# Optimization experiments

Hardware: AMD Instinct MI355X
Metric: run time of the kernel (lower is better)

The kernel has to match this reference:

```python
import jax, jax.numpy as jnp
import numpy as np

B, S, D, H, DK, DFF, L = 4, 1024, 1024, 16, 64, 4096, 128

def setup_inputs() -> dict:
    key = jax.random.key(0)
    ks = jax.random.split(key, 20)
    stdv = 1.0 / np.sqrt(D)
    u = lambda k, shape, s=stdv: jax.random.uniform(k, shape, jnp.float32, -s, s)
    x = jax.random.normal(ks[0], (B, S, D), jnp.float32)
    causal = jnp.triu(jnp.ones((S, S), bool), 1)          # True = masked
    attn_mask = jnp.broadcast_to(causal, (B, S, S))
    return {
        "x": x,
        "attn_mask": attn_mask,
        "W_q": u(ks[1], (H * DK, D)), "b_q": jnp.zeros((H * DK,)),
        "W_k": u(ks[2], (H * DK, D)), "b_k": jnp.zeros((H * DK,)),
        "W_v": u(ks[3], (H * DK, D)), "b_v": jnp.zeros((H * DK,)),
        "W_o": u(ks[4], (D, H * DK)), "b_o": jnp.zeros((D,)),
        "W_rel": u(ks[5], (2 * L + 1, DK), 1.0 / np.sqrt(DK)),
        "ln1_alpha": jnp.ones((D,)), "ln1_bias": jnp.zeros((D,)),
        "ln2_alpha": jnp.ones((D,)), "ln2_bias": jnp.zeros((D,)),
        "W1": u(ks[6], (DFF, D)), "b1": jnp.zeros((DFF,)),
        "W2": u(ks[7], (D, DFF)), "b2": jnp.zeros((D,)),
    }

def _layer_norm(x, alpha, bias, eps=1e-5):
    # Faithful to source: (x - mean) / (std + eps), std is biased (unbiased=False)
    m = jnp.mean(x, axis=-1, keepdims=True)
    std = jnp.sqrt(jnp.mean((x - m) ** 2, axis=-1, keepdims=True))
    return alpha * (x - m) / (std + eps) + bias

def reference(x, attn_mask, W_q, b_q, W_k, b_k, W_v, b_v, W_o, b_o, W_rel,
              ln1_alpha, ln1_bias, ln2_alpha, ln2_bias, W1, b1, W2, b2):
    b, s, d = x.shape
    q = (x @ W_q.T + b_q).reshape(b, s, H, DK)
    k = (x @ W_k.T + b_k).reshape(b, s, H, DK)
    v = (x @ W_v.T + b_v).reshape(b, s, H, DK)
    # relative position bias table lookup -> [s, s, DK]
    idx = jnp.clip(jnp.arange(s)[:, None] - jnp.arange(s)[None, :], -L, L) + L
    pos = W_rel[idx]
    # NOTE: original uses rel_pos_k_emb for BOTH pos_key and pos_value (as in source).
    scores = jnp.einsum('bqnd,bknd->bnqk', q, k) + jnp.einsum('bqnd,qkd->bnqk', q, pos)
    scores = scores / np.sqrt(DK)
    scores = jnp.where(attn_mask[:, None, :, :], jnp.float32(-10000.0), scores)
    attn = jax.nn.softmax(scores, axis=-1)
    out = jnp.einsum('bnqk,bknd->bnqd', attn, v) + jnp.einsum('bnqk,qkd->bnqd', attn, pos)
    out = out.transpose(0, 2, 1, 3).reshape(b, s, H * DK)
    out = out @ W_o.T + b_o
    # post-LN transformer layer: LN(x + attn), then LN(h + FFN(h))
    h = _layer_norm(x + out, ln1_alpha, ln1_bias)
    f = jax.nn.relu(h @ W1.T + b1) @ W2.T + b2
    return _layer_norm(h + f, ln2_alpha, ln2_bias)
```

## Files before the change

### kernel.cpp

```cpp
#include <hip/hip_runtime.h>
#include <cmath>
#include <cstdint>

typedef __bf16 bf16;
typedef __bf16 bf16x8 __attribute__((ext_vector_type(8)));
typedef __bf16 bf16x4 __attribute__((ext_vector_type(4)));
typedef float f32x4 __attribute__((ext_vector_type(4)));

#define CEXP 0.1803368852f

__device__ __forceinline__ void async_ld16(const void* g, void* l) {
  __builtin_amdgcn_global_load_lds(
      (__attribute__((address_space(1))) void*)(uintptr_t)g,
      (__attribute__((address_space(3))) void*)l, 16, 0, 0);
}

__global__ __launch_bounds__(256) void cast_all(
    const float* __restrict__ x,  const float* __restrict__ wq, const float* __restrict__ wk,
    const float* __restrict__ wv, const float* __restrict__ wo, const float* __restrict__ w1,
    const float* __restrict__ w2,
    bf16* xb, bf16* wqb, bf16* wkb, bf16* wvb, bf16* wob, bf16* w1b, bf16* w2b)
{
  int i = blockIdx.x * 256 + threadIdx.x;
  const int M1 = 1 << 20, Q = 1 << 18;
  const float* src; bf16* dst; int off;
  if      (i < M1)            { src = x;  dst = xb;  off = i; }
  else if (i < M1 + Q)        { src = wq; dst = wqb; off = i - M1; }
  else if (i < M1 + 2 * Q)    { src = wk; dst = wkb; off = i - M1 - Q; }
  else if (i < M1 + 3 * Q)    { src = wv; dst = wvb; off = i - M1 - 2 * Q; }
  else if (i < M1 + 4 * Q)    { src = wo; dst = wob; off = i - M1 - 3 * Q; }
  else if (i < 3 * M1)        { src = w1; dst = w1b; off = i - M1 - 4 * Q; }
  else                        { src = w2; dst = w2b; off = i - 3 * M1; }
  float4 v = ((const float4*)src)[off];
  bf16x4 o; o[0]=(bf16)v.x; o[1]=(bf16)v.y; o[2]=(bf16)v.z; o[3]=(bf16)v.w;
  ((bf16x4*)dst)[off] = o;
}

template<int BM>
__device__ __forceinline__ void gemm_core(
    const bf16* __restrict__ A, const bf16* __restrict__ Bm, const float* __restrict__ bias,
    float* __restrict__ outF, bf16* __restrict__ outB,
    const float* __restrict__ residF, const bf16* __restrict__ residB,
    int N, int kld, int kbeg, int kend, int relu, bf16* As, bf16* Bs)
{
  constexpr int MI = BM / 32;
  const int tid  = threadIdx.x;
  const int wave = tid >> 6, lane = tid & 63;
  const int lr = lane & 15, lq = lane >> 4;
  const int bm = blockIdx.x * BM, bn = blockIdx.y * 128;
  const int wm = (wave >> 1) * (BM / 2), wn = (wave & 1) * 64;
  const int srow = lane >> 2, scol = (lane & 3) * 8;

  const f32x4 fz = {0.f, 0.f, 0.f, 0.f};
  f32x4 acc[MI][4];
#pragma unroll
  for (int i = 0; i < MI; i++)
#pragma unroll
    for (int j = 0; j < 4; j++) acc[i][j] = fz;

  auto issue = [&](int k0, int buf) {
    bf16* Ad = As + buf * (BM * 32);
    bf16* Bd = Bs + buf * (128 * 32);
    if (BM == 128) {
#pragma unroll
      for (int cc = 0; cc < 2; ++cc) {
        int c = wave * 2 + cc;
        async_ld16(A + (size_t)(bm + c * 16 + srow) * kld + k0 + scol, Ad + c * 512);
      }
    } else {
      async_ld16(A + (size_t)(bm + wave * 16 + srow) * kld + k0 + scol, Ad + wave * 512);
    }
#pragma unroll
    for (int cc = 0; cc < 2; ++cc) {
      int c = wave * 2 + cc;
      async_ld16(Bm + (size_t)(bn + c * 16 + srow) * kld + k0 + scol, Bd + c * 512);
    }
  };

  const int nit = (kend - kbeg) >> 5;
  issue(kbeg, 0);
  for (int i = 0; i < nit; i++) {
    __syncthreads();
    if (i + 1 < nit) issue(kbeg + (i + 1) * 32, (i + 1) & 1);
    const bf16* Ab = As + (i & 1) * (BM * 32);
    const bf16* Bb = Bs + (i & 1) * (128 * 32);
    bf16x8 af[MI], bfr[4];
#pragma unroll
    for (int mi = 0; mi < MI; mi++) af[mi]  = *(const bf16x8*)(Ab + (wm + mi*16 + lr)*32 + lq*8);
#pragma unroll
    for (int ni = 0; ni < 4; ni++) bfr[ni] = *(const bf16x8*)(Bb + (wn + ni*16 + lr)*32 + lq*8);
#pragma unroll
    for (int mi = 0; mi < MI; mi++)
#pragma unroll
      for (int ni = 0; ni < 4; ni++)
        acc[mi][ni] = __builtin_amdgcn_mfma_f32_16x16x32_bf16(af[mi], bfr[ni], acc[mi][ni], 0, 0, 0);
  }

#pragma unroll
  for (int ni = 0; ni < 4; ni++) {
    int n = bn + wn + ni*16 + lr;
    float bv = bias ? bias[n] : 0.0f;
#pragma unroll
    for (int mi = 0; mi < MI; mi++) {
#pragma unroll
      for (int r = 0; r < 4; r++) {
        int m = bm + wm + mi*16 + lq*4 + r;
        size_t idx = (size_t)m * N + n;
        float v = acc[mi][ni][r] + bv;
        if (relu) v = fmaxf(v, 0.0f);
        if (residF) v += residF[idx];
        if (residB) v += (float)residB[idx];
        if (outF) outF[idx] = v;
        else      outB[idx] = (bf16)v;
      }
    }
  }
}

__global__ __launch_bounds__(256) void gemm_splitk(
    const bf16* A, const bf16* Bm, float* part, int N, int kld, int kchunk)
{
  __shared__ bf16 As[2 * 128 * 32];
  __shared__ bf16 Bs[2 * 128 * 32];
  const int z = blockIdx.z;
  gemm_core<128>(A, Bm, nullptr, part + (size_t)z * 4096 * N, nullptr, nullptr, nullptr,
                 N, kld, z * kchunk, (z + 1) * kchunk, 0, As, Bs);
}

__device__ __forceinline__ void gemm256_core(
    const bf16* __restrict__ A, const bf16* __restrict__ Bm,
    const float* __restrict__ bias, bf16* __restrict__ outB,
    int N, int K, int relu, bf16* As, bf16* Bs)
{
  const int tid  = threadIdx.x;
  const int wave = tid >> 6, lane = tid & 63;
  const int lr = lane & 15, lq = lane >> 4;
  const int bm = blockIdx.x * 256, bn = blockIdx.y * 256;
  const int wm = (wave >> 2) * 128, wn = (wave & 3) * 64;

  const f32x4 fz = {0.f, 0.f, 0.f, 0.f};
  f32x4 acc[8][4];
#pragma unroll
  for (int i = 0; i < 8; ++i)
#pragma unroll
    for (int j = 0; j < 4; ++j) acc[i][j] = fz;

  int srow[4], scol[4];
#pragma unroll
  for (int L = 0; L < 4; ++L) {
    int cidx = L * 512 + wave * 64 + lane;
    srow[L] = cidx >> 3;
    scol[L] = ((cidx & 7) ^ (srow[L] & 7)) * 8;
  }

  auto issue = [&](int kt, int buf) {
    const int k0 = kt * 64;
#pragma unroll
    for (int L = 0; L < 4; ++L)
      async_ld16(A + (size_t)(bm + srow[L]) * K + k0 + scol[L],
                 As + buf * (256 * 64) + (L * 512 + wave * 64) * 8);
#pragma unroll
    for (int L = 0; L < 4; ++L)
      async_ld16(Bm + (size_t)(bn + srow[L]) * K + k0 + scol[L],
                 Bs + buf * (256 * 64) + (L * 512 + wave * 64) * 8);
  };

  const int NT = K >> 6;
  issue(0, 0);
  issue(1, 1);
  asm volatile("s_waitcnt vmcnt(8)" ::: "memory");
  __builtin_amdgcn_sched_barrier(0);
  __builtin_amdgcn_s_barrier();

  for (int t = 0; t < NT; ++t) {
    const bf16* Ab = As + (t & 1) * (256 * 64);
    const bf16* Bb = Bs + (t & 1) * (256 * 64);
#pragma unroll
    for (int mh = 0; mh < 2; ++mh) {
      bf16x8 af[4][2];
#pragma unroll
      for (int mi = 0; mi < 4; ++mi) {
        int row = wm + mh * 64 + mi * 16 + lr;
#pragma unroll
        for (int ks = 0; ks < 2; ++ks)
          af[mi][ks] = *(const bf16x8*)(Ab + row * 64 + (((ks * 4 + lq) ^ (lr & 7)) * 8));
      }
#pragma unroll
      for (int nh = 0; nh < 2; ++nh) {
        bf16x8 bfr[2][2];
#pragma unroll
        for (int ni = 0; ni < 2; ++ni) {
          int row = wn + nh * 32 + ni * 16 + lr;
#pragma unroll
          for (int ks = 0; ks < 2; ++ks)
            bfr[ni][ks] = *(const bf16x8*)(Bb + row * 64 + (((ks * 4 + lq) ^ (lr & 7)) * 8));
        }
        __builtin_amdgcn_s_setprio(1);
#pragma unroll
        for (int mi = 0; mi < 4; ++mi)
#pragma unroll
          for (int ni = 0; ni < 2; ++ni)
#pragma unroll
            for (int ks = 0; ks < 2; ++ks)
              acc[mh * 4 + mi][nh * 2 + ni] = __builtin_amdgcn_mfma_f32_16x16x32_bf16(
                  af[mi][ks], bfr[ni][ks], acc[mh * 4 + mi][nh * 2 + ni], 0, 0, 0);
        __builtin_amdgcn_s_setprio(0);
      }
    }
    if (t + 1 == NT) break;
    asm volatile("s_waitcnt lgkmcnt(0)" ::: "memory");
    __builtin_amdgcn_sched_barrier(0);
    __builtin_amdgcn_s_barrier();
    if (t + 2 < NT) {
      issue(t + 2, t & 1);
      asm volatile("s_waitcnt vmcnt(8)" ::: "memory");
    } else {
      asm volatile("s_waitcnt vmcnt(0)" ::: "memory");
    }
    __builtin_amdgcn_sched_barrier(0);
    __builtin_amdgcn_s_barrier();
  }

#pragma unroll
  for (int mi8 = 0; mi8 < 8; ++mi8) {
#pragma unroll
    for (int ni4 = 0; ni4 < 4; ++ni4) {
      int n = bn + wn + ni4 * 16 + lr;
      float bv = bias ? bias[n] : 0.0f;
#pragma unroll
      for (int r = 0; r < 4; ++r) {
        int m = bm + wm + mi8 * 16 + lq * 4 + r;
        float v = acc[mi8][ni4][r] + bv;
        if (relu) v = fmaxf(v, 0.0f);
        outB[(size_t)m * N + n] = (bf16)v;
      }
    }
  }
}

__global__ __launch_bounds__(512) void gemm256(
    const bf16* __restrict__ A, const bf16* __restrict__ Bm,
    const float* __restrict__ bias, bf16* __restrict__ outB,
    int N, int K, int relu)
{
  __shared__ __align__(16) bf16 As[2 * 256 * 64];
  __shared__ __align__(16) bf16 Bs[2 * 256 * 64];
  gemm256_core(A, Bm, bias, outB, N, K, relu, As, Bs);
}

__global__ __launch_bounds__(512) void gemm256_qkv(
    const bf16* __restrict__ A, const bf16* __restrict__ Bq, const bf16* __restrict__ Bk,
    const bf16* __restrict__ Bv, const float* __restrict__ bq, const float* __restrict__ bk,
    const float* __restrict__ bv, bf16* Oq, bf16* Ok, bf16* Ov, int N, int K)
{
  __shared__ __align__(16) bf16 As[2 * 256 * 64];
  __shared__ __align__(16) bf16 Bs[2 * 256 * 64];
  const bf16* Bm  = blockIdx.z == 0 ? Bq : (blockIdx.z == 1 ? Bk : Bv);
  const float* bi = blockIdx.z == 0 ? bq : (blockIdx.z == 1 ? bk : bv);
  bf16* O         = blockIdx.z == 0 ? Oq : (blockIdx.z == 1 ? Ok : Ov);
  gemm256_core(A, Bm, bi, O, N, K, 0, As, Bs);
}

__global__ __launch_bounds__(256) void transpose_v(const bf16* __restrict__ V, bf16* __restrict__ Vt) {
  __shared__ bf16 t[64][72];
  const int tid = threadIdx.x;
  const int sblk = blockIdx.x;
  const int bh = blockIdx.y;
  const int b = bh >> 4, h = bh & 15;
  const int sr = tid >> 2, dc = (tid & 3) * 16;
  const bf16* src = V + ((size_t)(b * 1024 + sblk * 64 + sr)) * 1024 + h * 64 + dc;
  bf16x8 r0 = *(const bf16x8*)src;
  bf16x8 r1 = *(const bf16x8*)(src + 8);
  *(bf16x8*)(&t[sr][dc]) = r0;
  *(bf16x8*)(&t[sr][dc + 8]) = r1;
  __syncthreads();
  const int dr = tid >> 2, sc = (tid & 3) * 16;
  bf16 o[16];
#pragma unroll
  for (int j = 0; j < 16; j++) o[j] = t[sc + j][dr];
  bf16* dst = Vt + ((size_t)(bh * 64 + dr)) * 1024 + sblk * 64 + sc;
  *(bf16x8*)dst = *(bf16x8*)&o[0];
  *(bf16x8*)(dst + 8) = *(bf16x8*)&o[8];
}

#define S_LEN 1024
#define ROWSTR 1024

__global__ __launch_bounds__(256) void attn_kernel(
    const bf16* __restrict__ Qg, const bf16* __restrict__ Kg, const bf16* __restrict__ Vt,
    const float* __restrict__ Wrel, bf16* __restrict__ Og)
{
  __shared__ __align__(16) bf16 hist[64][136];
  __shared__ __align__(16) bf16 rel_s[64][132];
  __shared__ __align__(16) bf16 ovl[8704];
  bf16* V_T  = ovl;
  bf16* Pb   = ovl + 4096;
  bf16* Wst  = ovl;
  bf16* Wr_t = ovl;
  float* lbuf = (float*)rel_s;
  float* hbuf = lbuf + 256;

  const int tid = threadIdx.x;
  const int wave = tid >> 6, lane = tid & 63;
  const int lr = lane & 15, lq = lane >> 4;
  const int qblk = 15 - blockIdx.y;
  const int bh = blockIdx.x;
  const int b = bh >> 4, h = bh & 15;
  const int q0 = qblk * 64;
  const int T = qblk + 1;
  const int nearStart = (T > 3) ? T - 3 : 0;
  const size_t rowbase = (size_t)b * S_LEN * ROWSTR + h * 64;
  const size_t vtbase = (size_t)(bh * 64) * 1024;
  const f32x4 fz = {0.f, 0.f, 0.f, 0.f};

  for (int e = tid; e < 2048; e += 256) {
    float4 v = ((const float4*)(Wrel + 8192))[e];
    bf16x4 o; o[0]=(bf16)v.x; o[1]=(bf16)v.y; o[2]=(bf16)v.z; o[3]=(bf16)v.w;
    ((bf16x4*)Wst)[e] = o;
  }
  {
    uint4 z4 = {0u, 0u, 0u, 0u};
    for (int e = tid; e < 1088; e += 256) ((uint4*)hist)[e] = z4;
  }

  bf16x8 qf[4][2];
#pragma unroll
  for (int qt = 0; qt < 4; qt++)
#pragma unroll
    for (int c = 0; c < 2; c++)
      qf[qt][c] = *(const bf16x8*)(Qg + rowbase + (size_t)(q0 + qt*16 + lr) * ROWSTR + c*32 + lq*8);

  bf16x8 wb[2];
#pragma unroll
  for (int c = 0; c < 2; c++)
#pragma unroll
    for (int j = 0; j < 8; j++)
      wb[c][j] = (bf16)Wrel[(size_t)256 * 64 + c*32 + lq*8 + j];

  __syncthreads();

#pragma unroll
  for (int tt = 0; tt < 2; ++tt)
#pragma unroll
    for (int qt = 0; qt < 4; ++qt) {
      f32x4 a = fz;
#pragma unroll
      for (int c = 0; c < 2; c++) {
        bf16x8 wf = *(const bf16x8*)(Wst + (wave*32 + tt*16 + lr) * 64 + c*32 + lq*8);
        a = __builtin_amdgcn_mfma_f32_16x16x32_bf16(wf, qf[qt][c], a, 0, 0, 0);
      }
      bf16x4 pk; pk[0]=(bf16)(a[0]*CEXP); pk[1]=(bf16)(a[1]*CEXP);
                 pk[2]=(bf16)(a[2]*CEXP); pk[3]=(bf16)(a[3]*CEXP);
      *(bf16x4*)(&rel_s[qt*16 + lr][wave*32 + tt*16 + lq*4]) = pk;
    }
  {
    f32x4 a = fz;
#pragma unroll
    for (int c = 0; c < 2; c++)
      a = __builtin_amdgcn_mfma_f32_16x16x32_bf16(wb[c], qf[wave][c], a, 0, 0, 0);
    if (lq == 0) rel_s[wave*16 + lr][128] = (bf16)(a[0]*CEXP);
  }
  __syncthreads();

  float relc[4];
#pragma unroll
  for (int qt = 0; qt < 4; qt++) relc[qt] = (float)rel_s[qt*16 + lr][128];

  float l_p[4] = {0.f,0.f,0.f,0.f}, h_p[4] = {0.f,0.f,0.f,0.f};
  f32x4 acc_o[4];
#pragma unroll
  for (int dt = 0; dt < 4; dt++) acc_o[dt] = fz;

  const int vd1 = tid >> 3;
  const int vj  = (tid & 7) ^ (vd1 & 7);
  const int krow = 16 * wave + lr;

  uint4 va, vb, va2, vb2;
  bf16x8 kf0, kf1, kn0, kn1;
  {
    const bf16* vp = Vt + vtbase + (size_t)vd1 * 1024 + vj * 8;
    va = *(const uint4*)vp; vb = *(const uint4*)(vp + 32 * 1024);
    const bf16* kp = Kg + rowbase + (size_t)krow * ROWSTR + lq*8;
    kf0 = *(const bf16x8*)kp; kf1 = *(const bf16x8*)(kp + 32);
  }

  for (int kt = 0; kt < T; ++kt) {
    const int k0 = kt * 64;

    f32x4 sc[4];
#pragma unroll
    for (int qt = 0; qt < 4; qt++) {
      sc[qt] = __builtin_amdgcn_mfma_f32_16x16x32_bf16(kf0, qf[qt][0], fz, 0, 0, 0);
      sc[qt] = __builtin_amdgcn_mfma_f32_16x16x32_bf16(kf1, qf[qt][1], sc[qt], 0, 0, 0);
    }
    if (kt + 1 < T) {
      const bf16* vp = Vt + vtbase + (size_t)vd1 * 1024 + k0 + 64 + vj * 8;
      va2 = *(const uint4*)vp; vb2 = *(const uint4*)(vp + 32 * 1024);
      const bf16* kp = Kg + rowbase + (size_t)(k0 + 64 + krow) * ROWSTR + lq*8;
      kn0 = *(const bf16x8*)kp; kn1 = *(const bf16x8*)(kp + 32);
    }

    float pw[4][4];
    if (kt < nearStart) {
#pragma unroll
      for (int qt = 0; qt < 4; qt++) {
#pragma unroll
        for (int r = 0; r < 4; r++) pw[qt][r] = exp2f(fmaf(sc[qt][r], CEXP, relc[qt]));
        float s4 = pw[qt][0] + pw[qt][1] + pw[qt][2] + pw[qt][3];
        l_p[qt] += s4; h_p[qt] += s4;
      }
    } else {
#pragma unroll
      for (int qt = 0; qt < 4; qt++) {
        int qg = q0 + qt*16 + lr;
#pragma unroll
        for (int r = 0; r < 4; r++) {
          int kg = k0 + 16*wave + lq*4 + r;
          float p = 0.0f;
          if (kg <= qg) {
            int t = qg - kg; int tc = t > 128 ? 128 : t;
            p = exp2f(fmaf(sc[qt][r], CEXP, (float)rel_s[qt*16 + lr][tc]));
            l_p[qt] += p;
            if (t >= 128) h_p[qt] += p;
            else          hist[qt*16 + lr][t] = (bf16)p;
          }
          pw[qt][r] = p;
        }
      }
    }

    __syncthreads();
    *(uint4*)(V_T + tid * 8) = va;
    *(uint4*)(V_T + (tid + 256) * 8) = vb;
#pragma unroll
    for (int qt = 0; qt < 4; qt++) {
      bf16x4 pk; pk[0]=(bf16)pw[qt][0]; pk[1]=(bf16)pw[qt][1];
                 pk[2]=(bf16)pw[qt][2]; pk[3]=(bf16)pw[qt][3];
      *(bf16x4*)(Pb + (qt*16 + lr) * 72 + 16*wave + lq*4) = pk;
    }
    __syncthreads();

#pragma unroll
    for (int c = 0; c < 2; c++) {
      bf16x8 pf = *(const bf16x8*)(Pb + (16*wave + lr) * 72 + c*32 + lq*8);
#pragma unroll
      for (int dt = 0; dt < 4; dt++) {
        int vd = dt*16 + lr;
        int jx = (c*4 + lq) ^ (vd & 7);
        bf16x8 vf = *(const bf16x8*)(V_T + ((vd << 3) + jx) * 8);
        acc_o[dt] = __builtin_amdgcn_mfma_f32_16x16x32_bf16(pf, vf, acc_o[dt], 0, 0, 0);
      }
    }
    kf0 = kn0; kf1 = kn1; va = va2; vb = vb2;
  }

#pragma unroll
  for (int qt = 0; qt < 4; qt++) {
    l_p[qt] += __shfl_xor(l_p[qt], 16); l_p[qt] += __shfl_xor(l_p[qt], 32);
    h_p[qt] += __shfl_xor(h_p[qt], 16); h_p[qt] += __shfl_xor(h_p[qt], 32);
  }
  __syncthreads();
  if (lq == 0) {
#pragma unroll
    for (int qt = 0; qt < 4; qt++) {
      lbuf[wave*64 + qt*16 + lr] = l_p[qt];
      hbuf[wave*64 + qt*16 + lr] = h_p[qt];
    }
  }
  for (int e = tid; e < 64 * 128; e += 256) {
    int d = e >> 7, t = e & 127;
    Wr_t[d * 136 + t] = (bf16)Wrel[(size_t)(128 + t) * 64 + d];
  }
  __syncthreads();
#pragma unroll
  for (int c = 0; c < 4; c++) {
    bf16x8 hf = *(const bf16x8*)&hist[wave*16 + lr][c*32 + lq*8];
#pragma unroll
    for (int dt = 0; dt < 4; dt++) {
      bf16x8 wf = *(const bf16x8*)(Wr_t + (dt*16 + lr) * 136 + c*32 + lq*8);
      acc_o[dt] = __builtin_amdgcn_mfma_f32_16x16x32_bf16(hf, wf, acc_o[dt], 0, 0, 0);
    }
  }
  float l4[4], h4[4];
#pragma unroll
  for (int r = 0; r < 4; r++) {
    int q = wave*16 + lq*4 + r;
    l4[r] = lbuf[q] + lbuf[64+q] + lbuf[128+q] + lbuf[192+q];
    h4[r] = hbuf[q] + hbuf[64+q] + hbuf[128+q] + hbuf[192+q];
  }
#pragma unroll
  for (int dt = 0; dt < 4; dt++) {
    float wv = Wrel[(size_t)256 * 64 + dt*16 + lr];
#pragma unroll
    for (int r = 0; r < 4; r++) acc_o[dt][r] += h4[r] * wv;
  }
#pragma unroll
  for (int dt = 0; dt < 4; dt++)
#pragma unroll
    for (int r = 0; r < 4; r++) {
      int qg = q0 + wave*16 + lq*4 + r;
      Og[rowbase + (size_t)qg * ROWSTR + dt*16 + lr] = (bf16)(acc_o[dt][r] / l4[r]);
    }
}

__global__ __launch_bounds__(256) void ln_fuse(
    const float* __restrict__ pA, const float* __restrict__ pB,
    const float* __restrict__ bias,
    const float* __restrict__ residF, const bf16* __restrict__ residB,
    const float* __restrict__ alpha, const float* __restrict__ beta,
    float* __restrict__ outF, bf16* __restrict__ outB)
{
  const int row = blockIdx.x, tid = threadIdx.x;
  const int lane = tid & 63, wave = tid >> 6;
  const size_t base = (size_t)row * 1024;
  float4 v = ((const float4*)(pA + base))[tid];
  float4 v2 = ((const float4*)(pB + base))[tid];
  v.x += v2.x; v.y += v2.y; v.z += v2.z; v.w += v2.w;
  float4 bv = ((const float4*)bias)[tid];
  v.x += bv.x; v.y += bv.y; v.z += bv.z; v.w += bv.w;
  if (residF) {
    float4 rv = ((const float4*)(residF + base))[tid];
    v.x += rv.x; v.y += rv.y; v.z += rv.z; v.w += rv.w;
  }
  if (residB) {
    bf16x4 rv = ((const bf16x4*)(residB + base))[tid];
    v.x += (float)rv[0]; v.y += (float)rv[1]; v.z += (float)rv[2]; v.w += (float)rv[3];
  }
  float s  = v.x + v.y + v.z + v.w;
  float ss = v.x*v.x + v.y*v.y + v.z*v.z + v.w*v.w;
#pragma unroll
  for (int off = 32; off; off >>= 1) { s += __shfl_down(s, off); ss += __shfl_down(ss, off); }
  __shared__ float rs[4], rss[4];
  if (lane == 0) { rs[wave] = s; rss[wave] = ss; }
  __syncthreads();
  s  = rs[0] + rs[1] + rs[2] + rs[3];
  ss = rss[0] + rss[1] + rss[2] + rss[3];
  float mean = s * (1.0f / 1024.0f);
  float var  = ss * (1.0f / 1024.0f) - mean * mean;
  float inv  = 1.0f / (sqrtf(fmaxf(var, 0.0f)) + 1e-5f);
  float4 a = ((const float4*)alpha)[tid];
  float4 bb = ((const float4*)beta)[tid];
  float o0 = a.x * (v.x - mean) * inv + bb.x;
  float o1 = a.y * (v.y - mean) * inv + bb.y;
  float o2 = a.z * (v.z - mean) * inv + bb.z;
  float o3 = a.w * (v.w - mean) * inv + bb.w;
  if (outF) { float4 o = {o0, o1, o2, o3}; ((float4*)(outF + base))[tid] = o; }
  if (outB) { bf16x4 o; o[0]=(bf16)o0; o[1]=(bf16)o1; o[2]=(bf16)o2; o[3]=(bf16)o3;
              ((bf16x4*)(outB + base))[tid] = o; }
}

extern "C" void kernel_launch(void* const* d_in, const int* in_sizes, int n_in,
                              void* d_out, int out_size, void* d_ws, size_t ws_size,
                              hipStream_t stream) {
  (void)in_sizes; (void)n_in; (void)out_size; (void)ws_size;
  const int D = 1024, DFF = 4096;

  const float* x    = (const float*)d_in[0];
  const float* Wq   = (const float*)d_in[2];
  const float* bq   = (const float*)d_in[3];
  const float* Wk   = (const float*)d_in[4];
  const float* bk   = (const float*)d_in[5];
  const float* Wv   = (const float*)d_in[6];
  const float* bv   = (const float*)d_in[7];
  const float* Wo   = (const float*)d_in[8];
  const float* bo   = (const float*)d_in[9];
  const float* Wrel = (const float*)d_in[10];
  const float* g1   = (const float*)d_in[11];
  const float* be1  = (const float*)d_in[12];
  const float* g2   = (const float*)d_in[13];
  const float* be2  = (const float*)d_in[14];
  const float* W1   = (const float*)d_in[15];
  const float* b1   = (const float*)d_in[16];
  const float* W2   = (const float*)d_in[17];
  const float* b2   = (const float*)d_in[18];

  char* ws = (char*)d_ws;
  const size_t MB = 1024 * 1024;
  bf16*  xb   = (bf16*)(ws + 0);
  bf16*  Wqb  = (bf16*)(ws + 8  * MB);
  bf16*  Wkb  = (bf16*)(ws + 10 * MB);
  bf16*  Wvb  = (bf16*)(ws + 12 * MB);
  bf16*  Wob  = (bf16*)(ws + 14 * MB);
  bf16*  W1b  = (bf16*)(ws + 16 * MB);
  bf16*  W2b  = (bf16*)(ws + 24 * MB);
  bf16*  Qb   = (bf16*)(ws + 32 * MB);
  bf16*  Kb   = (bf16*)(ws + 40 * MB);
  bf16*  Vb   = (bf16*)(ws + 48 * MB);
  bf16*  Vt   = (bf16*)(ws + 56 * MB);
  bf16*  AOb  = (bf16*)(ws + 48 * MB);
  float* part = (float*)(ws + 64 * MB);
  bf16*  f1   = Qb;
  bf16*  hb   = xb;

  cast_all<<<16384, 256, 0, stream>>>(x, Wq, Wk, Wv, Wo, W1, W2,
                                      xb, Wqb, Wkb, Wvb, Wob, W1b, W2b);

  gemm256_qkv<<<dim3(16, 4, 3), 512, 0, stream>>>(xb, Wqb, Wkb, Wvb, bq, bk, bv, Qb, Kb, Vb, D, D);
  transpose_v<<<dim3(16, 64), 256, 0, stream>>>(Vb, Vt);
  attn_kernel<<<dim3(64, 16), 256, 0, stream>>>(Qb, Kb, Vt, Wrel, AOb);
  gemm_splitk<<<dim3(32, 8, 2), 256, 0, stream>>>(AOb, Wob, part, D, D, 512);
  ln_fuse<<<4096, 256, 0, stream>>>(part, part + 4096 * 1024, bo, x, nullptr, g1, be1, nullptr, hb);
  gemm256<<<dim3(16, 16), 512, 0, stream>>>(hb, W1b, b1, f1, DFF, D, 1);
  gemm_splitk<<<dim3(32, 8, 2), 256, 0, stream>>>(f1, W2b, part, D, DFF, 2048);
  ln_fuse<<<4096, 256, 0, stream>>>(part, part + 4096 * 1024, b2, nullptr, hb, g2, be2, (float*)d_out, nullptr);
}
```

Baseline: 389.8 us.

## Use 256-tile split-K for FFN down-projection and 128-tile GEMM for QKV

The FFN second GEMM moves from a 128-tile 2-way split-K to a 256x256-tile 4-way split-K. Its fp32 partials go to four buffers, reusing dead workspace regions and the output buffer, and the LayerNorm kernel now sums all four. The QKV projection switches from 256x256 tiles (192 blocks) to the 128-tile core (768 blocks) to fill more compute units. The trade-off is more partial-sum traffic and aliasing of workspace and output memory, which is safe only if those regions are dead at that point.

Result: faster. 375.7 us (-3.6%).

```diff
diff --git a/kernel.cpp b/kernel.cpp
--- a/kernel.cpp
+++ b/kernel.cpp
@@ -127,10 +127,23 @@
                  N, kld, z * kchunk, (z + 1) * kchunk, 0, As, Bs);
 }
 
+__global__ __launch_bounds__(256) void gemm_qkv(
+    const bf16* A, const bf16* Bq, const bf16* Bk, const bf16* Bv,
+    const float* bq, const float* bk, const float* bv,
+    bf16* Oq, bf16* Ok, bf16* Ov, int N, int K)
+{
+  __shared__ bf16 As[2 * 128 * 32];
+  __shared__ bf16 Bs[2 * 128 * 32];
+  const bf16* Bm  = blockIdx.z == 0 ? Bq : (blockIdx.z == 1 ? Bk : Bv);
+  const float* bi = blockIdx.z == 0 ? bq : (blockIdx.z == 1 ? bk : bv);
+  bf16* O         = blockIdx.z == 0 ? Oq : (blockIdx.z == 1 ? Ok : Ov);
+  gemm_core<128>(A, Bm, bi, nullptr, O, nullptr, nullptr, N, K, 0, K, 0, As, Bs);
+}
+
 __device__ __forceinline__ void gemm256_core(
     const bf16* __restrict__ A, const bf16* __restrict__ Bm,
-    const float* __restrict__ bias, bf16* __restrict__ outB,
-    int N, int K, int relu, bf16* As, bf16* Bs)
+    const float* __restrict__ bias, bf16* __restrict__ outB, float* __restrict__ outF,
+    int N, int kld, int kbeg, int kend, int relu, bf16* As, bf16* Bs)
 {
   const int tid  = threadIdx.x;
   const int wave = tid >> 6, lane = tid & 63;
@@ -154,18 +167,18 @@
   }
 
   auto issue = [&](int kt, int buf) {
-    const int k0 = kt * 64;
+    const int k0 = kbeg + kt * 64;
 #pragma unroll
     for (int L = 0; L < 4; ++L)
-      async_ld16(A + (size_t)(bm + srow[L]) * K + k0 + scol[L],
+      async_ld16(A + (size_t)(bm + srow[L]) * kld + k0 + scol[L],
                  As + buf * (256 * 64) + (L * 512 + wave * 64) * 8);
 #pragma unroll
     for (int L = 0; L < 4; ++L)
-      async_ld16(Bm + (size_t)(bn + srow[L]) * K + k0 + scol[L],
+      async_ld16(Bm + (size_t)(bn + srow[L]) * kld + k0 + scol[L],
                  Bs + buf * (256 * 64) + (L * 512 + wave * 64) * 8);
   };
 
-  const int NT = K >> 6;
+  const int NT = (kend - kbeg) >> 6;
   issue(0, 0);
   issue(1, 1);
   asm volatile("s_waitcnt vmcnt(8)" ::: "memory");
@@ -230,9 +243,11 @@
 #pragma unroll
       for (int r = 0; r < 4; ++r) {
         int m = bm + wm + mi8 * 16 + lq * 4 + r;
+        size_t idx = (size_t)m * N + n;
         float v = acc[mi8][ni4][r] + bv;
         if (relu) v = fmaxf(v, 0.0f);
-        outB[(size_t)m * N + n] = (bf16)v;
+        if (outF) outF[idx] = v;
+        else      outB[idx] = (bf16)v;
       }
     }
   }
@@ -245,20 +260,19 @@
 {
   __shared__ __align__(16) bf16 As[2 * 256 * 64];
   __shared__ __align__(16) bf16 Bs[2 * 256 * 64];
-  gemm256_core(A, Bm, bias, outB, N, K, relu, As, Bs);
-}
-
-__global__ __launch_bounds__(512) void gemm256_qkv(
-    const bf16* __restrict__ A, const bf16* __restrict__ Bq, const bf16* __restrict__ Bk,
-    const bf16* __restrict__ Bv, const float* __restrict__ bq, const float* __restrict__ bk,
-    const float* __restrict__ bv, bf16* Oq, bf16* Ok, bf16* Ov, int N, int K)
+  gemm256_core(A, Bm, bias, outB, nullptr, N, K, 0, K, relu, As, Bs);
+}
+
+__global__ __launch_bounds__(512) void gemm256_splitk(
+    const bf16* __restrict__ A, const bf16* __restrict__ Bm,
+    float* p0, float* p1, float* p2, float* p3,
+    int N, int kld, int kchunk)
 {
   __shared__ __align__(16) bf16 As[2 * 256 * 64];
   __shared__ __align__(16) bf16 Bs[2 * 256 * 64];
-  const bf16* Bm  = blockIdx.z == 0 ? Bq : (blockIdx.z == 1 ? Bk : Bv);
-  const float* bi = blockIdx.z == 0 ? bq : (blockIdx.z == 1 ? bk : bv);
-  bf16* O         = blockIdx.z == 0 ? Oq : (blockIdx.z == 1 ? Ok : Ov);
-  gemm256_core(A, Bm, bi, O, N, K, 0, As, Bs);
+  const int z = blockIdx.z;
+  float* part = z == 0 ? p0 : (z == 1 ? p1 : (z == 2 ? p2 : p3));
+  gemm256_core(A, Bm, nullptr, nullptr, part, N, kld, z * kchunk, (z + 1) * kchunk, 0, As, Bs);
 }
 
 __global__ __launch_bounds__(256) void transpose_v(const bf16* __restrict__ V, bf16* __restrict__ Vt) {
@@ -505,6 +519,7 @@
 
 __global__ __launch_bounds__(256) void ln_fuse(
     const float* __restrict__ pA, const float* __restrict__ pB,
+    const float* __restrict__ pC, const float* __restrict__ pD,
     const float* __restrict__ bias,
     const float* __restrict__ residF, const bf16* __restrict__ residB,
     const float* __restrict__ alpha, const float* __restrict__ beta,
@@ -516,6 +531,14 @@
   float4 v = ((const float4*)(pA + base))[tid];
   float4 v2 = ((const float4*)(pB + base))[tid];
   v.x += v2.x; v.y += v2.y; v.z += v2.z; v.w += v2.w;
+  if (pC) {
+    float4 v3 = ((const float4*)(pC + base))[tid];
+    v.x += v3.x; v.y += v3.y; v.z += v3.z; v.w += v3.w;
+  }
+  if (pD) {
+    float4 v4 = ((const float4*)(pD + base))[tid];
+    v.x += v4.x; v.y += v4.y; v.z += v4.z; v.w += v4.w;
+  }
   float4 bv = ((const float4*)bias)[tid];
   v.x += bv.x; v.y += bv.y; v.z += bv.z; v.w += bv.w;
   if (residF) {
@@ -591,16 +614,22 @@
   float* part = (float*)(ws + 64 * MB);
   bf16*  f1   = Qb;
   bf16*  hb   = xb;
+  float* f2p0 = (float*)(ws + 64 * MB);
+  float* f2p1 = (float*)(ws + 80 * MB);
+  float* f2p2 = (float*)(ws + 8 * MB);
+  float* f2p3 = (float*)d_out;
 
   cast_all<<<16384, 256, 0, stream>>>(x, Wq, Wk, Wv, Wo, W1, W2,
                                       xb, Wqb, Wkb, Wvb, Wob, W1b, W2b);
 
-  gemm256_qkv<<<dim3(16, 4, 3), 512, 0, stream>>>(xb, Wqb, Wkb, Wvb, bq, bk, bv, Qb, Kb, Vb, D, D);
+  gemm_qkv<<<dim3(32, 8, 3), 256, 0, stream>>>(xb, Wqb, Wkb, Wvb, bq, bk, bv, Qb, Kb, Vb, D, D);
   transpose_v<<<dim3(16, 64), 256, 0, stream>>>(Vb, Vt);
   attn_kernel<<<dim3(64, 16), 256, 0, stream>>>(Qb, Kb, Vt, Wrel, AOb);
   gemm_splitk<<<dim3(32, 8, 2), 256, 0, stream>>>(AOb, Wob, part, D, D, 512);
-  ln_fuse<<<4096, 256, 0, stream>>>(part, part + 4096 * 1024, bo, x, nullptr, g1, be1, nullptr, hb);
+  ln_fuse<<<4096, 256, 0, stream>>>(part, part + 4096 * 1024, nullptr, nullptr,
+                                    bo, x, nullptr, g1, be1, nullptr, hb);
   gemm256<<<dim3(16, 16), 512, 0, stream>>>(hb, W1b, b1, f1, DFF, D, 1);
-  gemm_splitk<<<dim3(32, 8, 2), 256, 0, stream>>>(f1, W2b, part, D, DFF, 2048);
-  ln_fuse<<<4096, 256, 0, stream>>>(part, part + 4096 * 1024, b2, nullptr, hb, g2, be2, (float*)d_out, nullptr);
-}
+  gemm256_splitk<<<dim3(16, 4, 4), 512, 0, stream>>>(f1, W2b, f2p0, f2p1, f2p2, f2p3, D, DFF, 1024);
+  ln_fuse<<<4096, 256, 0, stream>>>(f2p0, f2p1, f2p2, f2p3,
+                                    b2, nullptr, hb, g2, be2, (float*)d_out, nullptr);
+}
```
